# Kernel optimization log

Measured on AMD Instinct MI355X. Metric: run time of the kernel, lower is better.

Reference implementation:

```python
import jax, jax.numpy as jnp
import numpy as np

B, L, H, HS, OUT = 4, 512, 768, 64, 16  # batch, seq_len, hidden, head_size, output_size


def setup_inputs() -> dict:
    key = jax.random.key(0)
    ks = jax.random.split(key, 4)
    return {
        "x": jax.random.normal(ks[0], (B, L, H), dtype=jnp.float32),
        "Wq": jax.random.normal(ks[1], (H, HS), dtype=jnp.float32) * 0.02,
        "bq": jnp.zeros((HS,), dtype=jnp.float32),
        "Wk": jax.random.normal(ks[2], (H, HS), dtype=jnp.float32) * 0.02,
        "bk": jnp.zeros((HS,), dtype=jnp.float32),
        "Wb": jax.random.normal(ks[3], (4 * HS, OUT), dtype=jnp.float32) * 0.02,
        "bb": jnp.zeros((OUT,), dtype=jnp.float32),
    }


def _tri_indices(seq_len):
    # pair p corresponds to (start=i, end=j) with j >= i, ordered by i then j
    idx_start = np.repeat(np.arange(seq_len), np.arange(seq_len, 0, -1))
    idx_end = np.concatenate([np.arange(i, seq_len) for i in range(seq_len)])
    return idx_start, idx_end


def reference(x, Wq, bq, Wk, bk, Wb, bb):
    seq_len = x.shape[1]
    idx_start, idx_end = _tri_indices(seq_len)  # static numpy, P = L*(L+1)/2

    # Project per-token first (math-equivalent to projecting the gathered
    # pair tensors, since Linear is applied token-wise), then gather pairs.
    q = x @ Wq + bq  # [B, L, HS]
    k = x @ Wk + bk  # [B, L, HS]

    q_start = q[:, idx_start]  # query(start_token_hidden)  [B, P, HS]
    q_end = q[:, idx_end]      # query(end_token_hidden)
    k_end = k[:, idx_end]      # key(end_token_hidden) == key_start == key_end

    # entity_type_bias(cat([query_start, key_start, query_end, key_end]))
    feat = jnp.concatenate([q_start, k_end, q_end, k_end], axis=-1) @ Wb + bb  # [B, P, OUT]

    # einsum('blnh,blnh->bln') with n=1 -> per-pair dot product, broadcast over OUT
    score = jnp.einsum('bph,bph->bp', q_start, k_end)[..., None]  # [B, P, 1]
    return score + feat  # [B, P, OUT]
```

## Files before the change

kernel.cpp:

```cpp
#include <hip/hip_runtime.h>
#include <hip/hip_bf16.h>

#define Bc   4
#define Lc   512
#define Hc   768
#define HSc  64
#define OUTc 16
#define Pc   131328
#define KC   128
#define NCH  6

typedef float floatx4 __attribute__((ext_vector_type(4)));
typedef short bf16x8  __attribute__((ext_vector_type(8)));
typedef float f32x4   __attribute__((ext_vector_type(4)));


__device__ __forceinline__ unsigned short f2bf(float f) {
    unsigned int u = __float_as_uint(f);
    return (unsigned short)((u + 0x7FFFu + ((u >> 16) & 1u)) >> 16);
}

#define XPITCH 776
#define WPITCH 136

__global__ __launch_bounds__(256) void proj_kernel(
    const float* __restrict__ x,
    const float* __restrict__ Wq, const float* __restrict__ bq,
    const float* __restrict__ Wk, const float* __restrict__ bk,
    const float* __restrict__ Wb, const float* __restrict__ bb,
    float* __restrict__ qws, float* __restrict__ kws,
    float* __restrict__ Aws, float* __restrict__ Eqws, float* __restrict__ Ekws)
{
    __shared__ __align__(16) char lds_raw[16 * XPITCH * 2 + 64 * WPITCH * 2];
    unsigned short* lx = (unsigned short*)lds_raw;
    unsigned short* lw = (unsigned short*)(lds_raw + 16 * XPITCH * 2);
    float* lc = (float*)(lds_raw + 16 * XPITCH * 2);

    const int tid  = threadIdx.x;
    const int bx   = blockIdx.x;
    const int mb   = bx >> 1;
    const int nh   = bx & 1;
    const int m0   = mb * 16;
    const int w    = tid >> 6;
    const int lane = tid & 63;
    const int l15  = lane & 15;
    const int quad = lane >> 4;

    {
        const float4* xg = (const float4*)(x + (size_t)m0 * Hc);
        #pragma unroll
        for (int i = 0; i < 12; ++i) {
            const int flat = tid + i * 256;
            const int row  = flat / 192;
            const int c4   = flat - row * 192;
            const float4 v = xg[flat];
            ushort4 o = make_ushort4(f2bf(v.x), f2bf(v.y), f2bf(v.z), f2bf(v.w));
            *(ushort4*)&lx[row * XPITCH + c4 * 4] = o;
        }
    }

    const float* Ws = nh ? Wk : Wq;
    f32x4 acc = {0.f, 0.f, 0.f, 0.f};

    for (int c = 0; c < NCH; ++c) {
        const int k0 = c * KC;
        if (c) __syncthreads();
        #pragma unroll 4
        for (int i = 0; i < 16; ++i) {
            const int slot = tid + i * 256;
            const int n  = slot & 63;
            const int kp = slot >> 6;
            const float w0 = Ws[(k0 + 2 * kp) * HSc + n];
            const float w1 = Ws[(k0 + 2 * kp + 1) * HSc + n];
            const unsigned int pk = (unsigned)f2bf(w0) | ((unsigned)f2bf(w1) << 16);
            *(unsigned int*)&lw[n * WPITCH + 2 * kp] = pk;
        }
        __syncthreads();
        #pragma unroll
        for (int m = 0; m < 4; ++m) {
            const int ko = m * 32 + quad * 8;
            const bf16x8 a = *(const bf16x8*)&lx[l15 * XPITCH + k0 + ko];
            const bf16x8 b = *(const bf16x8*)&lw[(w * 16 + l15) * WPITCH + ko];
            acc = __builtin_amdgcn_mfma_f32_16x16x32_bf16(a, b, acc, 0, 0, 0);
        }
    }
    __syncthreads();

    const int gcol = w * 16 + l15;
    const float bias = nh ? bk[gcol] : bq[gcol];
    float* dst = nh ? kws : qws;
    #pragma unroll
    for (int r = 0; r < 4; ++r) {
        const int tl = quad * 4 + r;
        const float v = acc[r] + bias;
        dst[(size_t)(m0 + tl) * HSc + gcol] = v;
        lc[tl * 64 + gcol] = v;
    }
    __syncthreads();

    if (nh == 0) {
        #pragma unroll
        for (int i = 0; i < 2; ++i) {
            const int slot = tid + i * 256;
            const int t  = slot >> 5;
            const int cc = slot & 31;
            const float* row = &lc[t * 64];
            const int tok = m0 + t;
            if (cc < 16) {
                float a = 0.f;
                #pragma unroll 8
                for (int h = 0; h < 64; ++h) a += row[h] * Wb[h * OUTc + cc];
                Aws[(size_t)tok * OUTc + cc] = a;
            } else {
                const int o = cc - 16;
                float ev = 0.f;
                #pragma unroll 8
                for (int h = 0; h < 64; ++h) ev += row[h] * Wb[(128 + h) * OUTc + o];
                Eqws[(size_t)tok * OUTc + o] = ev;
            }
        }
    } else {
        const int t = tid >> 4;
        const int o = tid & 15;
        const float* row = &lc[t * 64];
        const int tok = m0 + t;
        float ev = bb[o];
        #pragma unroll 8
        for (int h = 0; h < 64; ++h)
            ev += row[h] * (Wb[(64 + h) * OUTc + o] + Wb[(192 + h) * OUTc + o]);
        Ekws[(size_t)tok * OUTc + o] = ev;
    }
}

__global__ __launch_bounds__(256) void pair_kernel(
    const float* __restrict__ qws, const float* __restrict__ kws,
    const float* __restrict__ Aws, const float* __restrict__ Eqws,
    const float* __restrict__ Ekws, float* __restrict__ out)
{
    const int j = blockIdx.x;
    const int i = blockIdx.y;
    const int b = blockIdx.z;
    if (j < (i >> 2)) return;

    __shared__ alignas(16) float q_tile[16][64];
    __shared__ alignas(16) float A_tile[16][16];

    const int tid = threadIdx.x;
    const int s0 = i * 16;
    const int e0 = j * 64;

    {
        const int r = tid >> 4, c4 = tid & 15;
        ((float4*)q_tile[r])[c4] =
            ((const float4*)(qws + ((size_t)b * Lc + s0 + r) * HSc))[c4];
        if (tid < 64) {
            const int ra = tid >> 2, ca = tid & 3;
            ((float4*)A_tile[ra])[ca] =
                ((const float4*)(Aws + ((size_t)b * Lc + s0 + ra) * OUTc))[ca];
        }
    }
    __syncthreads();

    const int g = tid >> 2;
    const int l = tid & 3;
    const int e = e0 + g;

    const float4* kk = (const float4*)(kws + ((size_t)b * Lc + e) * HSc);
    const float4 kv0 = kk[l];
    const float4 kv1 = kk[4 + l];
    const float4 kv2 = kk[8 + l];
    const float4 kv3 = kk[12 + l];
    const float4 e1 = ((const float4*)(Eqws + ((size_t)b * Lc + e) * OUTc))[l];
    const float4 e2 = ((const float4*)(Ekws + ((size_t)b * Lc + e) * OUTc))[l];
    const float4 ev = make_float4(e1.x + e2.x, e1.y + e2.y, e1.z + e2.z, e1.w + e2.w);

    float* ob = out + (size_t)b * Pc * OUTc;

    #pragma unroll 8
    for (int sl = 0; sl < 16; ++sl) {
        const int s = s0 + sl;
        const float4* qq = (const float4*)q_tile[sl];
        const float4 qv0 = qq[l];
        const float4 qv1 = qq[4 + l];
        const float4 qv2 = qq[8 + l];
        const float4 qv3 = qq[12 + l];

        float sc = qv0.x * kv0.x + qv0.y * kv0.y + qv0.z * kv0.z + qv0.w * kv0.w
                 + qv1.x * kv1.x + qv1.y * kv1.y + qv1.z * kv1.z + qv1.w * kv1.w
                 + qv2.x * kv2.x + qv2.y * kv2.y + qv2.z * kv2.z + qv2.w * kv2.w
                 + qv3.x * kv3.x + qv3.y * kv3.y + qv3.z * kv3.z + qv3.w * kv3.w;
        sc += __shfl_xor(sc, 1);
        sc += __shfl_xor(sc, 2);

        if (e >= s) {
            const float4 av = ((const float4*)A_tile[sl])[l];
            const int row = s * (2 * Lc + 1 - s) / 2 + (e - s);
            floatx4 r;
            r.x = av.x + ev.x + sc;
            r.y = av.y + ev.y + sc;
            r.z = av.z + ev.z + sc;
            r.w = av.w + ev.w + sc;
            __builtin_nontemporal_store(r, (floatx4*)(ob + (size_t)row * OUTc) + l);
        }
    }
}

extern "C" void kernel_launch(void* const* d_in, const int* in_sizes, int n_in,
                              void* d_out, int out_size, void* d_ws, size_t ws_size,
                              hipStream_t stream) {
    const float* x  = (const float*)d_in[0];
    const float* Wq = (const float*)d_in[1];
    const float* bq = (const float*)d_in[2];
    const float* Wk = (const float*)d_in[3];
    const float* bk = (const float*)d_in[4];
    const float* Wb = (const float*)d_in[5];
    const float* bb = (const float*)d_in[6];

    float* ws   = (float*)d_ws;
    float* qws  = ws;
    float* kws  = ws + 131072;
    float* Aws  = ws + 262144;
    float* Eqws = ws + 294912;
    float* Ekws = ws + 327680;

    proj_kernel<<<dim3(256), dim3(256), 0, stream>>>(
        x, Wq, bq, Wk, bk, Wb, bb, qws, kws, Aws, Eqws, Ekws);
    pair_kernel<<<dim3(8, 32, 4), dim3(256), 0, stream>>>(
        qws, kws, Aws, Eqws, Ekws, (float*)d_out);
}
```

Before: 101.8 us.

## Fuse projection and pair kernels into one cooperative kernel with grid sync

Merges the projection and pair-output kernels into a single cooperative launch of 512 blocks. The first 256 blocks run the projection, then all blocks wait on a grid-wide barrier before walking a compacted list of the 576 valid upper-triangular tiles. This removes the second launch and the blocks that exited immediately in the old 3D grid. In exchange it adds grid-sync cost, leaves half the blocks idle during the projection, and makes some blocks handle two tiles in the pair phase.

```diff
diff --git a/kernel.cpp b/kernel.cpp
--- a/kernel.cpp
+++ b/kernel.cpp
@@ -1,5 +1,8 @@
 #include <hip/hip_runtime.h>
 #include <hip/hip_bf16.h>
+#include <hip/hip_cooperative_groups.h>
+
+namespace cg = cooperative_groups;
 
 #define Bc   4
 #define Lc   512
@@ -9,198 +12,207 @@
 #define Pc   131328
 #define KC   128
 #define NCH  6
+#define XPITCH 776
+#define WPITCH 136
 
 typedef float floatx4 __attribute__((ext_vector_type(4)));
 typedef short bf16x8  __attribute__((ext_vector_type(8)));
 typedef float f32x4   __attribute__((ext_vector_type(4)));
-
 
 __device__ __forceinline__ unsigned short f2bf(float f) {
     unsigned int u = __float_as_uint(f);
     return (unsigned short)((u + 0x7FFFu + ((u >> 16) & 1u)) >> 16);
 }
 
-#define XPITCH 776
-#define WPITCH 136
-
-__global__ __launch_bounds__(256) void proj_kernel(
+__global__ __launch_bounds__(256) void fused_kernel(
     const float* __restrict__ x,
     const float* __restrict__ Wq, const float* __restrict__ bq,
     const float* __restrict__ Wk, const float* __restrict__ bk,
     const float* __restrict__ Wb, const float* __restrict__ bb,
     float* __restrict__ qws, float* __restrict__ kws,
-    float* __restrict__ Aws, float* __restrict__ Eqws, float* __restrict__ Ekws)
+    float* __restrict__ Aws, float* __restrict__ Eqws, float* __restrict__ Ekws,
+    float* __restrict__ out)
 {
     __shared__ __align__(16) char lds_raw[16 * XPITCH * 2 + 64 * WPITCH * 2];
-    unsigned short* lx = (unsigned short*)lds_raw;
-    unsigned short* lw = (unsigned short*)(lds_raw + 16 * XPITCH * 2);
-    float* lc = (float*)(lds_raw + 16 * XPITCH * 2);
-
-    const int tid  = threadIdx.x;
-    const int bx   = blockIdx.x;
-    const int mb   = bx >> 1;
-    const int nh   = bx & 1;
-    const int m0   = mb * 16;
-    const int w    = tid >> 6;
-    const int lane = tid & 63;
-    const int l15  = lane & 15;
-    const int quad = lane >> 4;
-
-    {
-        const float4* xg = (const float4*)(x + (size_t)m0 * Hc);
+
+    const int tid = threadIdx.x;
+    const int bx  = blockIdx.x;
+
+    if (bx < 256) {
+        unsigned short* lx = (unsigned short*)lds_raw;
+        unsigned short* lw = (unsigned short*)(lds_raw + 16 * XPITCH * 2);
+        float* lc = (float*)(lds_raw + 16 * XPITCH * 2);
+
+        const int mb   = bx >> 1;
+        const int nh   = bx & 1;
+        const int m0   = mb * 16;
+        const int w    = tid >> 6;
+        const int lane = tid & 63;
+        const int l15  = lane & 15;
+        const int quad = lane >> 4;
+
+        {
+            const float4* xg = (const float4*)(x + (size_t)m0 * Hc);
+            #pragma unroll
+            for (int i = 0; i < 12; ++i) {
+                const int flat = tid + i * 256;
+                const int row  = flat / 192;
+                const int c4   = flat - row * 192;
+                const float4 v = xg[flat];
+                ushort4 o = make_ushort4(f2bf(v.x), f2bf(v.y), f2bf(v.z), f2bf(v.w));
+                *(ushort4*)&lx[row * XPITCH + c4 * 4] = o;
+            }
+        }
+
+        const float* Ws = nh ? Wk : Wq;
+        f32x4 acc = {0.f, 0.f, 0.f, 0.f};
+
+        for (int c = 0; c < NCH; ++c) {
+            const int k0 = c * KC;
+            if (c) __syncthreads();
+            #pragma unroll 4
+            for (int i = 0; i < 16; ++i) {
+                const int slot = tid + i * 256;
+                const int n  = slot & 63;
+                const int kp = slot >> 6;
+                const float w0 = Ws[(k0 + 2 * kp) * HSc + n];
+                const float w1 = Ws[(k0 + 2 * kp + 1) * HSc + n];
+                const unsigned int pk = (unsigned)f2bf(w0) | ((unsigned)f2bf(w1) << 16);
+                *(unsigned int*)&lw[n * WPITCH + 2 * kp] = pk;
+            }
+            __syncthreads();
+            #pragma unroll
+            for (int m = 0; m < 4; ++m) {
+                const int ko = m * 32 + quad * 8;
+                const bf16x8 a = *(const bf16x8*)&lx[l15 * XPITCH + k0 + ko];
+                const bf16x8 b = *(const bf16x8*)&lw[(w * 16 + l15) * WPITCH + ko];
+                acc = __builtin_amdgcn_mfma_f32_16x16x32_bf16(a, b, acc, 0, 0, 0);
+            }
+        }
+        __syncthreads();
+
+        const int gcol = w * 16 + l15;
+        const float bias = nh ? bk[gcol] : bq[gcol];
+        float* dst = nh ? kws : qws;
         #pragma unroll
-        for (int i = 0; i < 12; ++i) {
-            const int flat = tid + i * 256;
-            const int row  = flat / 192;
-            const int c4   = flat - row * 192;
-            const float4 v = xg[flat];
-            ushort4 o = make_ushort4(f2bf(v.x), f2bf(v.y), f2bf(v.z), f2bf(v.w));
-            *(ushort4*)&lx[row * XPITCH + c4 * 4] = o;
-        }
-    }
-
-    const float* Ws = nh ? Wk : Wq;
-    f32x4 acc = {0.f, 0.f, 0.f, 0.f};
-
-    for (int c = 0; c < NCH; ++c) {
-        const int k0 = c * KC;
-        if (c) __syncthreads();
-        #pragma unroll 4
-        for (int i = 0; i < 16; ++i) {
-            const int slot = tid + i * 256;
-            const int n  = slot & 63;
-            const int kp = slot >> 6;
-            const float w0 = Ws[(k0 + 2 * kp) * HSc + n];
-            const float w1 = Ws[(k0 + 2 * kp + 1) * HSc + n];
-            const unsigned int pk = (unsigned)f2bf(w0) | ((unsigned)f2bf(w1) << 16);
-            *(unsigned int*)&lw[n * WPITCH + 2 * kp] = pk;
-        }
-        __syncthreads();
-        #pragma unroll
-        for (int m = 0; m < 4; ++m) {
-            const int ko = m * 32 + quad * 8;
-            const bf16x8 a = *(const bf16x8*)&lx[l15 * XPITCH + k0 + ko];
-            const bf16x8 b = *(const bf16x8*)&lw[(w * 16 + l15) * WPITCH + ko];
-            acc = __builtin_amdgcn_mfma_f32_16x16x32_bf16(a, b, acc, 0, 0, 0);
-        }
-    }
-    __syncthreads();
-
-    const int gcol = w * 16 + l15;
-    const float bias = nh ? bk[gcol] : bq[gcol];
-    float* dst = nh ? kws : qws;
-    #pragma unroll
-    for (int r = 0; r < 4; ++r) {
-        const int tl = quad * 4 + r;
-        const float v = acc[r] + bias;
-        dst[(size_t)(m0 + tl) * HSc + gcol] = v;
-        lc[tl * 64 + gcol] = v;
-    }
-    __syncthreads();
-
-    if (nh == 0) {
-        #pragma unroll
-        for (int i = 0; i < 2; ++i) {
-            const int slot = tid + i * 256;
-            const int t  = slot >> 5;
-            const int cc = slot & 31;
+        for (int r = 0; r < 4; ++r) {
+            const int tl = quad * 4 + r;
+            const float v = acc[r] + bias;
+            dst[(size_t)(m0 + tl) * HSc + gcol] = v;
+            lc[tl * 64 + gcol] = v;
+        }
+        __syncthreads();
+
+        if (nh == 0) {
+            #pragma unroll
+            for (int i = 0; i < 2; ++i) {
+                const int slot = tid + i * 256;
+                const int t  = slot >> 5;
+                const int cc = slot & 31;
+                const float* row = &lc[t * 64];
+                const int tok = m0 + t;
+                if (cc < 16) {
+                    float a = 0.f;
+                    #pragma unroll 8
+                    for (int h = 0; h < 64; ++h) a += row[h] * Wb[h * OUTc + cc];
+                    Aws[(size_t)tok * OUTc + cc] = a;
+                } else {
+                    const int o = cc - 16;
+                    float ev = 0.f;
+                    #pragma unroll 8
+                    for (int h = 0; h < 64; ++h) ev += row[h] * Wb[(128 + h) * OUTc + o];
+                    Eqws[(size_t)tok * OUTc + o] = ev;
+                }
+            }
+        } else {
+            const int t = tid >> 4;
+            const int o = tid & 15;
             const float* row = &lc[t * 64];
             const int tok = m0 + t;
-            if (cc < 16) {
-                float a = 0.f;
-                #pragma unroll 8
-                for (int h = 0; h < 64; ++h) a += row[h] * Wb[h * OUTc + cc];
-                Aws[(size_t)tok * OUTc + cc] = a;
-            } else {
-                const int o = cc - 16;
-                float ev = 0.f;
-                #pragma unroll 8
-                for (int h = 0; h < 64; ++h) ev += row[h] * Wb[(128 + h) * OUTc + o];
-                Eqws[(size_t)tok * OUTc + o] = ev;
-            }
-        }
-    } else {
-        const int t = tid >> 4;
-        const int o = tid & 15;
-        const float* row = &lc[t * 64];
-        const int tok = m0 + t;
-        float ev = bb[o];
+            float ev = bb[o];
+            #pragma unroll 8
+            for (int h = 0; h < 64; ++h)
+                ev += row[h] * (Wb[(64 + h) * OUTc + o] + Wb[(192 + h) * OUTc + o]);
+            Ekws[(size_t)tok * OUTc + o] = ev;
+        }
+    }
+
+    __threadfence();
+    cg::this_grid().sync();
+
+    float* q_tile = (float*)lds_raw;
+    float* A_tile = (float*)(lds_raw + 4096);
+
+    const int cum[9] = {0, 32, 60, 84, 104, 120, 132, 140, 144};
+
+    for (int t = bx; t < 576; t += 512) {
+        const int b = t / 144;
+        const int r = t - b * 144;
+        int g = 0;
+        #pragma unroll
+        for (int h = 1; h < 8; ++h) if (r >= cum[h]) g = h;
+        const int local = r - cum[g];
+        const int njg = 8 - g;
+        const int iq  = local / njg;
+        const int i = 4 * g + iq;
+        const int j = g + (local - iq * njg);
+        const int s0 = i * 16;
+        const int e0 = j * 64;
+
+        __syncthreads();
+        {
+            const int rr = tid >> 4, c4 = tid & 15;
+            ((float4*)(q_tile + rr * 64))[c4] =
+                ((const float4*)(qws + ((size_t)b * Lc + s0 + rr) * HSc))[c4];
+            if (tid < 64) {
+                const int ra = tid >> 2, ca = tid & 3;
+                ((float4*)(A_tile + ra * 16))[ca] =
+                    ((const float4*)(Aws + ((size_t)b * Lc + s0 + ra) * OUTc))[ca];
+            }
+        }
+        __syncthreads();
+
+        const int gg = tid >> 2;
+        const int l  = tid & 3;
+        const int e  = e0 + gg;
+
+        const float4* kk = (const float4*)(kws + ((size_t)b * Lc + e) * HSc);
+        const float4 kv0 = kk[l];
+        const float4 kv1 = kk[4 + l];
+        const float4 kv2 = kk[8 + l];
+        const float4 kv3 = kk[12 + l];
+        const float4 e1 = ((const float4*)(Eqws + ((size_t)b * Lc + e) * OUTc))[l];
+        const float4 e2 = ((const float4*)(Ekws + ((size_t)b * Lc + e) * OUTc))[l];
+        const float4 ev = make_float4(e1.x + e2.x, e1.y + e2.y, e1.z + e2.z, e1.w + e2.w);
+
+        float* ob = out + (size_t)b * Pc * OUTc;
+
         #pragma unroll 8
-        for (int h = 0; h < 64; ++h)
-            ev += row[h] * (Wb[(64 + h) * OUTc + o] + Wb[(192 + h) * OUTc + o]);
-        Ekws[(size_t)tok * OUTc + o] = ev;
-    }
-}
-
-__global__ __launch_bounds__(256) void pair_kernel(
-    const float* __restrict__ qws, const float* __restrict__ kws,
-    const float* __restrict__ Aws, const float* __restrict__ Eqws,
-    const float* __restrict__ Ekws, float* __restrict__ out)
-{
-    const int j = blockIdx.x;
-    const int i = blockIdx.y;
-    const int b = blockIdx.z;
-    if (j < (i >> 2)) return;
-
-    __shared__ alignas(16) float q_tile[16][64];
-    __shared__ alignas(16) float A_tile[16][16];
-
-    const int tid = threadIdx.x;
-    const int s0 = i * 16;
-    const int e0 = j * 64;
-
-    {
-        const int r = tid >> 4, c4 = tid & 15;
-        ((float4*)q_tile[r])[c4] =
-            ((const float4*)(qws + ((size_t)b * Lc + s0 + r) * HSc))[c4];
-        if (tid < 64) {
-            const int ra = tid >> 2, ca = tid & 3;
-            ((float4*)A_tile[ra])[ca] =
-                ((const float4*)(Aws + ((size_t)b * Lc + s0 + ra) * OUTc))[ca];
-        }
-    }
-    __syncthreads();
-
-    const int g = tid >> 2;
-    const int l = tid & 3;
-    const int e = e0 + g;
-
-    const float4* kk = (const float4*)(kws + ((size_t)b * Lc + e) * HSc);
-    const float4 kv0 = kk[l];
-    const float4 kv1 = kk[4 + l];
-    const float4 kv2 = kk[8 + l];
-    const float4 kv3 = kk[12 + l];
-    const float4 e1 = ((const float4*)(Eqws + ((size_t)b * Lc + e) * OUTc))[l];
-    const float4 e2 = ((const float4*)(Ekws + ((size_t)b * Lc + e) * OUTc))[l];
-    const float4 ev = make_float4(e1.x + e2.x, e1.y + e2.y, e1.z + e2.z, e1.w + e2.w);
-
-    float* ob = out + (size_t)b * Pc * OUTc;
-
-    #pragma unroll 8
-    for (int sl = 0; sl < 16; ++sl) {
-        const int s = s0 + sl;
-        const float4* qq = (const float4*)q_tile[sl];
-        const float4 qv0 = qq[l];
-        const float4 qv1 = qq[4 + l];
-        const float4 qv2 = qq[8 + l];
-        const float4 qv3 = qq[12 + l];
-
-        float sc = qv0.x * kv0.x + qv0.y * kv0.y + qv0.z * kv0.z + qv0.w * kv0.w
-                 + qv1.x * kv1.x + qv1.y * kv1.y + qv1.z * kv1.z + qv1.w * kv1.w
-                 + qv2.x * kv2.x + qv2.y * kv2.y + qv2.z * kv2.z + qv2.w * kv2.w
-                 + qv3.x * kv3.x + qv3.y * kv3.y + qv3.z * kv3.z + qv3.w * kv3.w;
-        sc += __shfl_xor(sc, 1);
-        sc += __shfl_xor(sc, 2);
-
-        if (e >= s) {
-            const float4 av = ((const float4*)A_tile[sl])[l];
-            const int row = s * (2 * Lc + 1 - s) / 2 + (e - s);
-            floatx4 r;
-            r.x = av.x + ev.x + sc;
-            r.y = av.y + ev.y + sc;
-            r.z = av.z + ev.z + sc;
-            r.w = av.w + ev.w + sc;
-            __builtin_nontemporal_store(r, (floatx4*)(ob + (size_t)row * OUTc) + l);
+        for (int sl = 0; sl < 16; ++sl) {
+            const int s = s0 + sl;
+            const float4* qq = (const float4*)(q_tile + sl * 64);
+            const float4 qv0 = qq[l];
+            const float4 qv1 = qq[4 + l];
+            const float4 qv2 = qq[8 + l];
+            const float4 qv3 = qq[12 + l];
+
+            float sc = qv0.x * kv0.x + qv0.y * kv0.y + qv0.z * kv0.z + qv0.w * kv0.w
+                     + qv1.x * kv1.x + qv1.y * kv1.y + qv1.z * kv1.z + qv1.w * kv1.w
+                     + qv2.x * kv2.x + qv2.y * kv2.y + qv2.z * kv2.z + qv2.w * kv2.w
+                     + qv3.x * kv3.x + qv3.y * kv3.y + qv3.z * kv3.z + qv3.w * kv3.w;
+            sc += __shfl_xor(sc, 1);
+            sc += __shfl_xor(sc, 2);
+
+            if (e >= s) {
+                const float4 av = ((const float4*)(A_tile + sl * 16))[l];
+                const int row = s * (2 * Lc + 1 - s) / 2 + (e - s);
+                floatx4 rr;
+                rr.x = av.x + ev.x + sc;
+                rr.y = av.y + ev.y + sc;
+                rr.z = av.z + ev.z + sc;
+                rr.w = av.w + ev.w + sc;
+                __builtin_nontemporal_store(rr, (floatx4*)(ob + (size_t)row * OUTc) + l);
+            }
         }
     }
 }
@@ -222,9 +234,13 @@
     float* Aws  = ws + 262144;
     float* Eqws = ws + 294912;
     float* Ekws = ws + 327680;
-
-    proj_kernel<<<dim3(256), dim3(256), 0, stream>>>(
-        x, Wq, bq, Wk, bk, Wb, bb, qws, kws, Aws, Eqws, Ekws);
-    pair_kernel<<<dim3(8, 32, 4), dim3(256), 0, stream>>>(
-        qws, kws, Aws, Eqws, Ekws, (float*)d_out);
+    float* outp = (float*)d_out;
+
+    void* args[] = {
+        (void*)&x, (void*)&Wq, (void*)&bq, (void*)&Wk, (void*)&bk,
+        (void*)&Wb, (void*)&bb, (void*)&qws, (void*)&kws,
+        (void*)&Aws, (void*)&Eqws, (void*)&Ekws, (void*)&outp
+    };
+    hipLaunchCooperativeKernel(fused_kernel, dim3(512), dim3(256),
+                               args, 0, stream);
 }
```

Result: slower. 216.5 us (+112.7%).
